# Kernel optimization log

Measured on AMD Instinct MI355X. Metric: run time of the kernel, lower is better.

## Reference

```python
import jax, jax.numpy as jnp
import numpy as np

EMB = 1024
FF = 4 * EMB

def _ternary(w):
    # BitNet b1.58 absmean quantization; forward uses pure ternary weights
    scale = jnp.maximum(jnp.mean(jnp.abs(w)), 1e-8)
    w_t = jnp.clip(jnp.round(w / scale), -1.0, 1.0)
    # STE: forward = w_t, backward = identity w.r.t. w
    return w + jax.lax.stop_gradient(w_t - w)

def setup_inputs() -> dict:
    key = jax.random.key(0)
    kx, k1, k2, kb1, kb2 = jax.random.split(key, 5)
    x = jax.random.normal(kx, (4, 2048, EMB), dtype=jnp.float32)
    # nn.Linear default init: U(-1/sqrt(fan_in), 1/sqrt(fan_in))
    lim1 = 1.0 / np.sqrt(EMB)
    lim2 = 1.0 / np.sqrt(FF)
    W1 = jax.random.uniform(k1, (FF, EMB), jnp.float32, -lim1, lim1)
    b1 = jax.random.uniform(kb1, (FF,), jnp.float32, -lim1, lim1)
    W2 = jax.random.uniform(k2, (EMB, FF), jnp.float32, -lim2, lim2)
    b2 = jax.random.uniform(kb2, (EMB,), jnp.float32, -lim2, lim2)
    return {"x": x, "W1": W1, "b1": b1, "W2": W2, "b2": b2}

def reference(x, W1, b1, W2, b2):
    h = jnp.einsum('bsd,fd->bsf', x, _ternary(W1)) + b1  # [B,S,FF]
    h = jax.nn.gelu(h, approximate=False)  # torch nn.GELU default = exact erf
    out = jnp.einsum('bsf,df->bsd', h, _ternary(W2)) + b2  # [B,S,EMB]
    return out
```

## Files before the change

kernel.cpp:

```cpp
#include <hip/hip_runtime.h>
#include <hip/hip_bf16.h>
#include <cstdint>
#include <cstddef>

typedef __bf16 bf16x8 __attribute__((ext_vector_type(8)));
typedef float  f32x4  __attribute__((ext_vector_type(4)));

__device__ __forceinline__ unsigned short f2bf(float f) {
    __hip_bfloat16 b = __float2bfloat16(f);
    return *reinterpret_cast<unsigned short*>(&b);
}

__device__ __forceinline__ float fast_gelu(float x) {
    float x2 = x * x;
    float m  = x * __builtin_fmaf(x2, -0.10294314f, -2.30220795f);
    float e  = __builtin_amdgcn_exp2f(m);
    return x * __builtin_amdgcn_rcpf(1.0f + e);
}


__global__ void abs_sum_cvt_kernel(const float4* __restrict__ w0, const float4* __restrict__ w1,
                                   int n4w, float* __restrict__ part,
                                   const float4* __restrict__ x, ushort4* __restrict__ xb,
                                   int n4x) {
    int seg = (int)blockIdx.x >> 9;
    int b = (int)blockIdx.x & 511;
    if (seg == 2) {
        for (int i = b * blockDim.x + threadIdx.x; i < n4x; i += 512 * blockDim.x) {
            float4 v = x[i];
            ushort4 o;
            o.x = f2bf(v.x); o.y = f2bf(v.y); o.z = f2bf(v.z); o.w = f2bf(v.w);
            xb[i] = o;
        }
        return;
    }
    const float4* w = seg ? w1 : w0;
    float s = 0.0f;
    for (int i = b * blockDim.x + threadIdx.x; i < n4w; i += 512 * blockDim.x) {
        float4 v = w[i];
        s += fabsf(v.x) + fabsf(v.y) + fabsf(v.z) + fabsf(v.w);
    }
    #pragma unroll
    for (int o = 32; o > 0; o >>= 1) s += __shfl_down(s, o, 64);
    __shared__ float ps[4];
    int lane = threadIdx.x & 63, wid = threadIdx.x >> 6;
    if (lane == 0) ps[wid] = s;
    __syncthreads();
    if (threadIdx.x == 0) part[blockIdx.x] = ps[0] + ps[1] + ps[2] + ps[3];
}

__global__ void ternarize_kernel(const float4* __restrict__ w0, ushort4* __restrict__ t0,
                                 const float4* __restrict__ w1, ushort4* __restrict__ t1,
                                 int n4w, const float* __restrict__ part, float inv_n) {
    int seg = (int)blockIdx.x >> 10;
    int b = (int)blockIdx.x & 1023;

    float s = 0.0f;
    for (int j = threadIdx.x; j < 512; j += 256) s += part[seg * 512 + j];
    #pragma unroll
    for (int o = 32; o > 0; o >>= 1) s += __shfl_down(s, o, 64);
    __shared__ float ps[4];
    __shared__ float sscale;
    int lane = threadIdx.x & 63, wid = threadIdx.x >> 6;
    if (lane == 0) ps[wid] = s;
    __syncthreads();
    if (threadIdx.x == 0) {
        float tot = ps[0] + ps[1] + ps[2] + ps[3];
        sscale = fmaxf(tot * inv_n, 1e-8f);
    }
    __syncthreads();
    float inv = 1.0f / sscale;

    const float4* w = seg ? w1 : w0;
    ushort4* t = seg ? t1 : t0;
    for (int i = b * blockDim.x + threadIdx.x; i < n4w; i += 1024 * blockDim.x) {
        float4 v = w[i];
        ushort4 o;
        o.x = f2bf(fminf(fmaxf(rintf(v.x * inv), -1.0f), 1.0f));
        o.y = f2bf(fminf(fmaxf(rintf(v.y * inv), -1.0f), 1.0f));
        o.z = f2bf(fminf(fmaxf(rintf(v.z * inv), -1.0f), 1.0f));
        o.w = f2bf(fminf(fmaxf(rintf(v.w * inv), -1.0f), 1.0f));
        t[i] = o;
    }
}


#define GLL(SRC, DST) __builtin_amdgcn_global_load_lds( \
    (const __attribute__((address_space(1))) void*)(SRC), \
    (__attribute__((address_space(3))) void*)(DST), 16, 0, 0)

#define BAR() do { asm volatile("" ::: "memory"); \
    __builtin_amdgcn_sched_barrier(0); \
    __builtin_amdgcn_s_barrier(); \
    __builtin_amdgcn_sched_barrier(0); \
    asm volatile("" ::: "memory"); } while (0)

#define WLG0() do { asm volatile("s_waitcnt lgkmcnt(0)" ::: "memory"); \
    __builtin_amdgcn_sched_barrier(0); } while (0)
#define WVM_N(NN) do { asm volatile("s_waitcnt vmcnt(" #NN ")" ::: "memory"); \
    __builtin_amdgcn_sched_barrier(0); } while (0)
#define WVM_TILE() do { if constexpr (SBL == 2) WVM_N(6); else WVM_N(5); } while (0)

#define LDA(MS, BUF) do { \
    _Pragma("unroll") \
    for (int f_ = 0; f_ < MF2; ++f_) { \
        const unsigned short* p_ = &As[(BUF)*16384 + AH*8192 + (rA0 + (MS)*(WM/2) + f_*16 + lr)*64]; \
        av[MS][f_][0] = *(const bf16x8*)(p_ + swz0); \
        av[MS][f_][1] = *(const bf16x8*)(p_ + swz1); \
    } \
} while (0)

#define LDB(NS, BUF) do { \
    _Pragma("unroll") \
    for (int g_ = 0; g_ < NF2; ++g_) { \
        const unsigned short* p_ = &Bs[(BUF)*(BN*64) + BHw*(BH*64) + (rB0 + (NS)*32 + g_*16 + lr)*64]; \
        bv[NS][g_][0] = *(const bf16x8*)(p_ + swz0); \
        bv[NS][g_][1] = *(const bf16x8*)(p_ + swz1); \
    } \
} while (0)

#define MMA(MS, NS) do { \
    __builtin_amdgcn_s_setprio(1); \
    _Pragma("unroll") \
    for (int f_ = 0; f_ < MF2; ++f_) { \
        _Pragma("unroll") \
        for (int g_ = 0; g_ < NF2; ++g_) { \
            acc[(MS)*MF2 + f_][(NS)*NF2 + g_] = __builtin_amdgcn_mfma_f32_16x16x32_bf16( \
                av[MS][f_][0], bv[NS][g_][0], acc[(MS)*MF2 + f_][(NS)*NF2 + g_], 0, 0, 0); \
            acc[(MS)*MF2 + f_][(NS)*NF2 + g_] = __builtin_amdgcn_mfma_f32_16x16x32_bf16( \
                av[MS][f_][1], bv[NS][g_][1], acc[(MS)*MF2 + f_][(NS)*NF2 + g_], 0, 0, 0); \
        } \
    } \
    __builtin_amdgcn_s_setprio(0); \
} while (0)

#define STAGE_A(BUF, H, T) do { \
    const unsigned short* s_ = pA + (size_t)((H)*128)*K + (((T) & (KT-1)) << 6); \
    GLL(s_,                 &As[(BUF)*16384 + (H)*8192 + tid*8]); \
    GLL(s_ + (size_t)64*K,  &As[(BUF)*16384 + (H)*8192 + 4096 + tid*8]); \
} while (0)

#define STAGE_BH(BUF, H, T) do { \
    const unsigned short* s_ = pB + (size_t)((H)*BH)*K + (((T) & (KT-1)) << 6); \
    GLL(s_, &Bs[(BUF)*(BN*64) + (H)*(BH*64) + tid*8]); \
    if constexpr (BN == 256) { \
        GLL(s_ + (size_t)64*K, &Bs[(BUF)*(BN*64) + (H)*(BH*64) + 4096 + tid*8]); \
    } \
} while (0)

template <int EPI, int K, int N, int BN, int WM>
__global__ __launch_bounds__(512, 2)
void gemm8p_kernel(const unsigned short* __restrict__ A,
                   const unsigned short* __restrict__ B,
                   const float* __restrict__ bias,
                   void* __restrict__ C) {
    constexpr int BM = 256;
    constexpr int WN = 64;
    constexpr int WARPS_N = BN / WN;
    constexpr int MF = WM / 16;
    constexpr int NF = WN / 16;
    constexpr int MF2 = MF / 2;
    constexpr int NF2 = NF / 2;
    constexpr int BH = (BN == 256) ? 128 : 64;
    constexpr int SBL = (BN == 256) ? 2 : 1;
    constexpr int KT = K / 64;
    constexpr int NBX = N / BN;
    static_assert((BM / WM) * WARPS_N == 8, "8 waves");
    static_assert((KT & (KT - 1)) == 0, "KT pow2");

    __shared__ __align__(16) unsigned short As[2 * 256 * 64];
    __shared__ __align__(16) unsigned short Bs[2 * BN * 64];

    const int tid  = threadIdx.x;
    const int lane = tid & 63;
    const int wid  = tid >> 6;
    const int lr = lane & 15;
    const int lq = lane >> 4;
    const int mb = wid / WARPS_N;
    const int nb = wid % WARPS_N;

    const int nwg = (int)gridDim.x;
    const int bid = (int)blockIdx.x;
    const int swz = (bid & 7) * (nwg >> 3) + (bid >> 3);
    const int bx = swz % NBX;
    const int by = swz / NBX;
    const size_t aRow0 = (size_t)by * BM;
    const size_t bRow0 = (size_t)bx * BN;

    const int sRow = tid >> 3;
    const int sChunk = ((tid & 7) ^ (sRow & 7)) << 3;
    const unsigned short* pA = A + (aRow0 + sRow) * (size_t)K + sChunk;
    const unsigned short* pB = B + (bRow0 + sRow) * (size_t)K + sChunk;

    const int swz0 = ((lq ^ (lr & 7)) << 3);
    const int swz1 = (((4 + lq) ^ (lr & 7)) << 3);
    const int AH  = (mb * WM) >> 7;
    const int rA0 = (mb * WM) & 127;
    const int BHw = (nb * WN) / BH;
    const int rB0 = (nb * WN) % BH;

    f32x4 acc[MF][NF];
    #pragma unroll
    for (int i_ = 0; i_ < MF; ++i_)
        #pragma unroll
        for (int j_ = 0; j_ < NF; ++j_)
            acc[i_][j_] = f32x4{0.f, 0.f, 0.f, 0.f};

    bf16x8 av[2][MF2][2];
    bf16x8 bv[2][NF2][2];

    STAGE_A(0, 0, 0); STAGE_A(0, 1, 0); STAGE_BH(0, 0, 0); STAGE_BH(0, 1, 0);
    STAGE_A(1, 0, 1); STAGE_A(1, 1, 1); STAGE_BH(1, 0, 1);
    WVM_TILE();
    BAR();

    #pragma unroll 1
    for (int it = 0; it < K / 128; ++it) {
        const int t1 = 2 * it + 1;
        const int t2 = 2 * it + 2;
        const int t3 = 2 * it + 3;

        LDA(0, 0); LDB(0, 0);
        STAGE_BH(1, 1, t1);
        BAR(); WLG0();
        MMA(0, 0);
        BAR();

        LDA(1, 0);
        BAR(); WLG0();
        MMA(1, 0);
        BAR();

        LDB(1, 0);
        STAGE_A(0, 0, t2);
        BAR(); WLG0();
        MMA(1, 1);
        BAR();

        STAGE_A(0, 1, t2); STAGE_BH(0, 0, t2);
        BAR();
        MMA(0, 1);
        WVM_TILE();
        BAR();

        LDA(0, 1); LDB(0, 1);
        STAGE_BH(0, 1, t2);
        BAR(); WLG0();
        MMA(0, 0);
        BAR();

        LDA(1, 1);
        BAR(); WLG0();
        MMA(1, 0);
        BAR();

        LDB(1, 1);
        STAGE_A(1, 0, t3);
        BAR(); WLG0();
        MMA(1, 1);
        BAR();

        STAGE_A(1, 1, t3); STAGE_BH(1, 0, t3);
        BAR();
        MMA(0, 1);
        WVM_TILE();
        BAR();
    }

    WVM_N(0);

    #pragma unroll
    for (int mf = 0; mf < MF; ++mf) {
        #pragma unroll
        for (int nf = 0; nf < NF; ++nf) {
            const size_t col = bRow0 + (size_t)nb * WN + nf * 16 + lr;
            const float bvs = bias[col];
            #pragma unroll
            for (int r = 0; r < 4; ++r) {
                const size_t row = aRow0 + (size_t)mb * WM + mf * 16 + lq * 4 + r;
                float v = acc[mf][nf][r] + bvs;
                if constexpr (EPI == 0) {
                    ((unsigned short*)C)[row * (size_t)N + col] = f2bf(fast_gelu(v));
                } else {
                    ((float*)C)[row * (size_t)N + col] = v;
                }
            }
        }
    }
}

#undef GLL
#undef BAR
#undef WLG0
#undef WVM_N
#undef WVM_TILE
#undef LDA
#undef LDB
#undef MMA
#undef STAGE_A
#undef STAGE_BH


extern "C" void kernel_launch(void* const* d_in, const int* in_sizes, int n_in,
                              void* d_out, int out_size, void* d_ws, size_t ws_size,
                              hipStream_t stream) {
    const float* x  = (const float*)d_in[0];
    const float* W1 = (const float*)d_in[1];
    const float* b1 = (const float*)d_in[2];
    const float* W2 = (const float*)d_in[3];
    const float* b2 = (const float*)d_in[4];
    float* out = (float*)d_out;

    const int M = 8192, EMB = 1024, FF = 4096;
    const int nW = FF * EMB;

    char* ws = (char*)d_ws;
    float* part = (float*)ws;
    unsigned short* W1t = (unsigned short*)(ws + 16384);
    unsigned short* W2t = W1t + (size_t)nW;
    unsigned short* xb  = W2t + (size_t)nW;
    unsigned short* h   = xb  + (size_t)M * EMB;

    abs_sum_cvt_kernel<<<1536, 256, 0, stream>>>((const float4*)W1, (const float4*)W2,
                                                 nW / 4, part,
                                                 (const float4*)x, (ushort4*)xb,
                                                 (M * EMB) / 4);
    ternarize_kernel<<<2048, 256, 0, stream>>>((const float4*)W1, (ushort4*)W1t,
                                               (const float4*)W2, (ushort4*)W2t,
                                               nW / 4, part, 1.0f / nW);

    gemm8p_kernel<0, 1024, 4096, 256, 128><<<dim3(512), dim3(512), 0, stream>>>(xb, W1t, b1, h);
    gemm8p_kernel<1, 4096, 1024, 128, 64><<<dim3(256), dim3(512), 0, stream>>>(h, W2t, b2, out);
}
```

Baseline: 258.0 us.

## Peel final GEMM iteration and merge staging phases to cut barriers

The main K loop now runs one iteration fewer, and the last iteration is peeled into an epilogue block that issues no further global-to-LDS prefetches. Before, the loop wrapped tile indices modulo KT and loaded redundant tiles at the end. Inside the loop, the third and fourth phases of each half are merged: all A/B staging is issued together, followed by two MMA groups under one barrier pair. This removes barriers and wasted loads, at the cost of less interleaving between staging and MFMA work.

```diff
diff --git a/kernel.cpp b/kernel.cpp
--- a/kernel.cpp
+++ b/kernel.cpp
@@ -135,13 +135,13 @@
 } while (0)
 
 #define STAGE_A(BUF, H, T) do { \
-    const unsigned short* s_ = pA + (size_t)((H)*128)*K + (((T) & (KT-1)) << 6); \
+    const unsigned short* s_ = pA + (size_t)((H)*128)*K + ((size_t)(T) << 6); \
     GLL(s_,                 &As[(BUF)*16384 + (H)*8192 + tid*8]); \
     GLL(s_ + (size_t)64*K,  &As[(BUF)*16384 + (H)*8192 + 4096 + tid*8]); \
 } while (0)
 
 #define STAGE_BH(BUF, H, T) do { \
-    const unsigned short* s_ = pB + (size_t)((H)*BH)*K + (((T) & (KT-1)) << 6); \
+    const unsigned short* s_ = pB + (size_t)((H)*BH)*K + ((size_t)(T) << 6); \
     GLL(s_, &Bs[(BUF)*(BN*64) + (H)*(BH*64) + tid*8]); \
     if constexpr (BN == 256) { \
         GLL(s_ + (size_t)64*K, &Bs[(BUF)*(BN*64) + (H)*(BH*64) + 4096 + tid*8]); \
@@ -166,7 +166,7 @@
     constexpr int KT = K / 64;
     constexpr int NBX = N / BN;
     static_assert((BM / WM) * WARPS_N == 8, "8 waves");
-    static_assert((KT & (KT - 1)) == 0, "KT pow2");
+    static_assert(KT >= 4 && (KT & 1) == 0, "even KT >= 4");
 
     __shared__ __align__(16) unsigned short As[2 * 256 * 64];
     __shared__ __align__(16) unsigned short Bs[2 * BN * 64];
@@ -215,7 +215,7 @@
     BAR();
 
     #pragma unroll 1
-    for (int it = 0; it < K / 128; ++it) {
+    for (int it = 0; it < K / 128 - 1; ++it) {
         const int t1 = 2 * it + 1;
         const int t2 = 2 * it + 2;
         const int t3 = 2 * it + 3;
@@ -232,14 +232,9 @@
         BAR();
 
         LDB(1, 0);
-        STAGE_A(0, 0, t2);
-        BAR(); WLG0();
-        MMA(1, 1);
-        BAR();
-
-        STAGE_A(0, 1, t2); STAGE_BH(0, 0, t2);
-        BAR();
-        MMA(0, 1);
+        STAGE_A(0, 0, t2); STAGE_A(0, 1, t2); STAGE_BH(0, 0, t2);
+        BAR(); WLG0();
+        MMA(1, 1); MMA(0, 1);
         WVM_TILE();
         BAR();
 
@@ -255,19 +250,45 @@
         BAR();
 
         LDB(1, 1);
-        STAGE_A(1, 0, t3);
-        BAR(); WLG0();
-        MMA(1, 1);
-        BAR();
-
-        STAGE_A(1, 1, t3); STAGE_BH(1, 0, t3);
-        BAR();
-        MMA(0, 1);
+        STAGE_A(1, 0, t3); STAGE_A(1, 1, t3); STAGE_BH(1, 0, t3);
+        BAR(); WLG0();
+        MMA(1, 1); MMA(0, 1);
         WVM_TILE();
         BAR();
     }
 
-    WVM_N(0);
+    {
+        LDA(0, 0); LDB(0, 0);
+        STAGE_BH(1, 1, KT - 1);
+        BAR(); WLG0();
+        MMA(0, 0);
+        BAR();
+
+        LDA(1, 0);
+        BAR(); WLG0();
+        MMA(1, 0);
+        BAR();
+
+        LDB(1, 0);
+        BAR(); WLG0();
+        MMA(1, 1); MMA(0, 1);
+        WVM_N(0);
+        BAR();
+
+        LDA(0, 1); LDB(0, 1);
+        BAR(); WLG0();
+        MMA(0, 0);
+        BAR();
+
+        LDA(1, 1);
+        BAR(); WLG0();
+        MMA(1, 0);
+        BAR();
+
+        LDB(1, 1);
+        BAR(); WLG0();
+        MMA(1, 1); MMA(0, 1);
+    }
 
     #pragma unroll
     for (int mf = 0; mf < MF; ++mf) {
```

Result: no change. 259.4 us (+0.6%).

## Restructure GEMM main loop with partial LDS waits and peeled epilogue

Applied to the files above, without the earlier changes.

Reworks the 8-phase GEMM K-loop so LDS fragment reads for the next MMA are issued before the current MMA. The loop now waits with partial lgkmcnt/vmcnt counts instead of full drains, cuts the barriers per iteration, and peels the last iteration so it issues no wrapped-around prefetches. The aim is more overlap between LDS reads, global-to-LDS staging and MFMA work. The cost is tighter reliance on hand-counted waitcnt values, which could cause races if a count is wrong.

```diff
diff --git a/kernel.cpp b/kernel.cpp
--- a/kernel.cpp
+++ b/kernel.cpp
@@ -95,11 +95,17 @@
     __builtin_amdgcn_sched_barrier(0); \
     asm volatile("" ::: "memory"); } while (0)
 
-#define WLG0() do { asm volatile("s_waitcnt lgkmcnt(0)" ::: "memory"); \
+#define WLG_N(NN) do { asm volatile("s_waitcnt lgkmcnt(" #NN ")" ::: "memory"); \
     __builtin_amdgcn_sched_barrier(0); } while (0)
 #define WVM_N(NN) do { asm volatile("s_waitcnt vmcnt(" #NN ")" ::: "memory"); \
     __builtin_amdgcn_sched_barrier(0); } while (0)
-#define WVM_TILE() do { if constexpr (SBL == 2) WVM_N(6); else WVM_N(5); } while (0)
+
+#define WLG_RA() do { if constexpr (MF2 == 4) WLG_N(8); else WLG_N(4); } while (0)
+#define WLG_RB() WLG_N(4)
+#define WVM_P2() WVM_N(2)
+#define WVM_P6() WVM_N(4)
+#define WVM_P7() do { if constexpr (SBL == 2) WVM_N(6); else WVM_N(5); } while (0)
+#define WVM_PRO() do { if constexpr (SBL == 2) WVM_N(8); else WVM_N(6); } while (0)
 
 #define LDA(MS, BUF) do { \
     _Pragma("unroll") \
@@ -135,13 +141,13 @@
 } while (0)
 
 #define STAGE_A(BUF, H, T) do { \
-    const unsigned short* s_ = pA + (size_t)((H)*128)*K + (((T) & (KT-1)) << 6); \
+    const unsigned short* s_ = pA + (size_t)((H)*128)*K + ((size_t)(T) << 6); \
     GLL(s_,                 &As[(BUF)*16384 + (H)*8192 + tid*8]); \
     GLL(s_ + (size_t)64*K,  &As[(BUF)*16384 + (H)*8192 + 4096 + tid*8]); \
 } while (0)
 
 #define STAGE_BH(BUF, H, T) do { \
-    const unsigned short* s_ = pB + (size_t)((H)*BH)*K + (((T) & (KT-1)) << 6); \
+    const unsigned short* s_ = pB + (size_t)((H)*BH)*K + ((size_t)(T) << 6); \
     GLL(s_, &Bs[(BUF)*(BN*64) + (H)*(BH*64) + tid*8]); \
     if constexpr (BN == 256) { \
         GLL(s_ + (size_t)64*K, &Bs[(BUF)*(BN*64) + (H)*(BH*64) + 4096 + tid*8]); \
@@ -166,7 +172,7 @@
     constexpr int KT = K / 64;
     constexpr int NBX = N / BN;
     static_assert((BM / WM) * WARPS_N == 8, "8 waves");
-    static_assert((KT & (KT - 1)) == 0, "KT pow2");
+    static_assert(KT >= 4 && (KT & 1) == 0, "even KT >= 4");
 
     __shared__ __align__(16) unsigned short As[2 * 256 * 64];
     __shared__ __align__(16) unsigned short Bs[2 * BN * 64];
@@ -210,64 +216,81 @@
     bf16x8 bv[2][NF2][2];
 
     STAGE_A(0, 0, 0); STAGE_A(0, 1, 0); STAGE_BH(0, 0, 0); STAGE_BH(0, 1, 0);
-    STAGE_A(1, 0, 1); STAGE_A(1, 1, 1); STAGE_BH(1, 0, 1);
-    WVM_TILE();
+    STAGE_A(1, 0, 1); STAGE_A(1, 1, 1); STAGE_BH(1, 0, 1); STAGE_BH(1, 1, 1);
+    WVM_PRO();
     BAR();
+    LDB(0, 0); LDA(0, 0);
 
     #pragma unroll 1
-    for (int it = 0; it < K / 128; ++it) {
-        const int t1 = 2 * it + 1;
+    for (int it = 0; it < KT / 2 - 1; ++it) {
         const int t2 = 2 * it + 2;
         const int t3 = 2 * it + 3;
 
-        LDA(0, 0); LDB(0, 0);
-        STAGE_BH(1, 1, t1);
-        BAR(); WLG0();
+        LDA(1, 0);
+        BAR(); WLG_RA();
         MMA(0, 0);
-        BAR();
-
+
+        LDB(1, 0); STAGE_A(0, 0, t2);
+        BAR(); WLG_RB();
+        MMA(1, 0);
+        WVM_P2(); BAR();
+
+        LDB(0, 1); STAGE_BH(0, 0, t2);
+        BAR(); WLG_RB();
+        MMA(1, 1);
+
+        LDA(1, 1); STAGE_BH(0, 1, t2);
+        BAR(); WLG_RA();
+        MMA(0, 1);
+
+        LDA(0, 1); STAGE_A(0, 1, t2);
+        BAR(); WLG_RA();
+        MMA(1, 0);
+
+        LDB(1, 1); STAGE_A(1, 0, t3);
+        BAR(); WLG_RB();
+        MMA(0, 0);
+        WVM_P6(); BAR();
+
+        LDB(0, 0); STAGE_A(1, 1, t3); STAGE_BH(1, 0, t3);
+        BAR(); WLG_RB();
+        MMA(0, 1);
+        WVM_P7(); BAR();
+
+        LDA(0, 0); STAGE_BH(1, 1, t3);
+        BAR(); WLG_RA();
+        MMA(1, 1);
+    }
+
+    {
         LDA(1, 0);
-        BAR(); WLG0();
+        BAR(); WLG_RA();
+        MMA(0, 0);
+
+        LDB(1, 0);
+        BAR(); WLG_RB();
         MMA(1, 0);
-        BAR();
-
-        LDB(1, 0);
-        STAGE_A(0, 0, t2);
-        BAR(); WLG0();
+        WVM_N(0); BAR();
+
+        LDB(0, 1);
+        BAR(); WLG_RB();
         MMA(1, 1);
-        BAR();
-
-        STAGE_A(0, 1, t2); STAGE_BH(0, 0, t2);
-        BAR();
+
+        LDA(1, 1);
+        BAR(); WLG_RA();
         MMA(0, 1);
-        WVM_TILE();
-        BAR();
-
-        LDA(0, 1); LDB(0, 1);
-        STAGE_BH(0, 1, t2);
-        BAR(); WLG0();
+
+        LDA(0, 1);
+        BAR(); WLG_RA();
+        MMA(1, 0);
+
+        LDB(1, 1);
+        BAR(); WLG_RB();
         MMA(0, 0);
-        BAR();
-
-        LDA(1, 1);
-        BAR(); WLG0();
-        MMA(1, 0);
-        BAR();
-
-        LDB(1, 1);
-        STAGE_A(1, 0, t3);
-        BAR(); WLG0();
-        MMA(1, 1);
-        BAR();
-
-        STAGE_A(1, 1, t3); STAGE_BH(1, 0, t3);
-        BAR();
-        MMA(0, 1);
-        WVM_TILE();
-        BAR();
-    }
-
-    WVM_N(0);
+
+        WLG_N(0);
+        MMA(0, 1); MMA(1, 1);
+    }
 
     #pragma unroll
     for (int mf = 0; mf < MF; ++mf) {
@@ -291,9 +314,14 @@
 
 #undef GLL
 #undef BAR
-#undef WLG0
+#undef WLG_N
 #undef WVM_N
-#undef WVM_TILE
+#undef WLG_RA
+#undef WLG_RB
+#undef WVM_P2
+#undef WVM_P6
+#undef WVM_P7
+#undef WVM_PRO
 #undef LDA
 #undef LDB
 #undef MMA
```

Result: slower. 269.8 us (+4.6%).
